# Optimization experiments

Hardware: AMD Instinct MI355X
Metric: run time of the kernel (lower is better)

## Reference

```python
import jax, jax.numpy as jnp
import numpy as np

B, C1, C2, K, H, W = 2, 256, 256, 3, 64, 64
PAD = 1
EPS = 1e-5
K2 = K * K
OUT_OFF = 3 * K2  # deform_groups=1: 2*k2 offset channels + k2 mask channels


def setup_inputs() -> dict:
    key = jax.random.key(0)
    ks = jax.random.split(key, 8)
    x = jax.random.normal(ks[0], (B, C1, H, W), jnp.float32)
    # small scale so predicted offsets stay within a few pixels (realistic trained regime)
    w_off = jax.random.normal(ks[1], (OUT_OFF, C1, 3, 3), jnp.float32) * 0.01
    b_off = jax.random.normal(ks[2], (OUT_OFF,), jnp.float32) * 0.01
    w_dcn = jax.random.normal(ks[3], (C2, C1, K, K), jnp.float32) / np.sqrt(C1 * K2).astype(np.float32)
    gamma = 1.0 + 0.1 * jax.random.normal(ks[4], (C2,), jnp.float32)
    beta = 0.1 * jax.random.normal(ks[5], (C2,), jnp.float32)
    run_mean = 0.1 * jax.random.normal(ks[6], (C2,), jnp.float32)
    run_var = jax.random.uniform(ks[7], (C2,), jnp.float32, minval=0.5, maxval=1.5)
    return {"x": x, "w_off": w_off, "b_off": b_off, "w_dcn": w_dcn,
            "gamma": gamma, "beta": beta, "run_mean": run_mean, "run_var": run_var}


def _dcnv2_bn_silu(x, w_off, b_off, w_dcn, gamma, beta, run_mean, run_var):
    # offset/mask predictor: plain 3x3 conv, stride 1, pad 1
    om = jax.lax.conv_general_dilated(x, w_off, (1, 1), [(PAD, PAD), (PAD, PAD)])
    om = om + b_off[None, :, None, None]  # [B, 27, H, W]
    # mmcv channel layout: (dy, dx) interleaved per kernel tap, then mask
    offset = om[:, :2 * K2].reshape(B, K2, 2, H, W)
    mask = jax.nn.sigmoid(om[:, 2 * K2:3 * K2])  # [B, K2, H, W]
    dy, dx = offset[:, :, 0], offset[:, :, 1]     # [B, K2, H, W]

    ki = jnp.arange(K)
    tap_y = jnp.repeat(ki, K)  # [K2]
    tap_x = jnp.tile(ki, K)    # [K2]
    base_y = jnp.arange(H)[None, None, :, None] - PAD + tap_y[None, :, None, None]
    base_x = jnp.arange(W)[None, None, None, :] - PAD + tap_x[None, :, None, None]
    py = base_y.astype(x.dtype) + dy  # [B, K2, H, W] sampling rows
    px = base_x.astype(x.dtype) + dx  # [B, K2, H, W] sampling cols

    y0f = jnp.floor(py)
    x0f = jnp.floor(px)
    ly = (py - y0f)[:, None]  # [B, 1, K2, H, W]
    lx = (px - x0f)[:, None]
    y0 = y0f.astype(jnp.int32)
    x0 = x0f.astype(jnp.int32)

    x_flat = x.reshape(B, C1, H * W)

    def gather(yi, xi):
        valid = ((yi >= 0) & (yi < H) & (xi >= 0) & (xi < W)).astype(x.dtype)
        idx = jnp.clip(yi, 0, H - 1) * W + jnp.clip(xi, 0, W - 1)  # [B, K2, H, W]
        v = jnp.take_along_axis(x_flat, idx.reshape(B, 1, -1), axis=2)
        return v.reshape(B, C1, K2, H, W) * valid[:, None]

    v00 = gather(y0, x0)
    v01 = gather(y0, x0 + 1)
    v10 = gather(y0 + 1, x0)
    v11 = gather(y0 + 1, x0 + 1)
    vals = (v00 * (1 - ly) * (1 - lx) + v01 * (1 - ly) * lx
            + v10 * ly * (1 - lx) + v11 * ly * lx)
    vals = vals * mask[:, None]  # modulated

    out = jnp.einsum('bckhw,ock->bohw', vals, w_dcn.reshape(C2, C1, K2))

    # BatchNorm (inference, running stats) + SiLU
    inv = gamma / jnp.sqrt(run_var + EPS)
    y = out * inv[None, :, None, None] + (beta - run_mean * inv)[None, :, None, None]
    return y * jax.nn.sigmoid(y)


def reference(x, w_off, b_off, w_dcn, gamma, beta, run_mean, run_var):
    return _dcnv2_bn_silu(x, w_off, b_off, w_dcn, gamma, beta, run_mean, run_var)
```

## Files before the change

kernel.cpp:

```cpp
#include <hip/hip_runtime.h>
#include <hip/hip_bf16.h>
#include <math.h>

typedef __bf16 bf16x8 __attribute__((ext_vector_type(8)));
typedef float  f32x4  __attribute__((ext_vector_type(4)));

#define BB 2
#define C1 256
#define C2 256
#define HH 64
#define WW 64
#define HW 4096
#define OCH 27
#define EPSV 1e-5f

#define OM_OFF   0u
#define WBF_OFF  884736u
#define WOFF_OFF 2064384u
#define XT_OFF   2211840u

__global__ __launch_bounds__(256) void xprep_kernel(
    const float* __restrict__ x, __bf16* __restrict__ xT)
{
    __shared__ __bf16 tile[64][72];

    const int bt = blockIdx.x;
    const int b = bt >> 8;
    const int ht = (bt & 255) >> 2;
    const int ct = bt & 3;
    const int tid = threadIdx.x;

    const int hw_l = tid & 63, cg = tid >> 6;
    const float* src = x + ((size_t)(b * 256 + ct * 64 + cg * 16) << 12) + ht * 64 + hw_l;
    #pragma unroll
    for (int i = 0; i < 16; i++)
        tile[hw_l][cg * 16 + i] = (__bf16)src[(size_t)i << 12];
    __syncthreads();

    const int hw_o = tid >> 2, cq = tid & 3;
    __bf16* dst = xT + ((size_t)(b * HW + ht * 64 + hw_o) << 8) + ct * 64 + cq * 16;
    *(bf16x8*)dst       = *(const bf16x8*)&tile[hw_o][cq * 16];
    *(bf16x8*)(dst + 8) = *(const bf16x8*)&tile[hw_o][cq * 16 + 8];
}

__global__ __launch_bounds__(256) void wprep_kernel(
    const float* __restrict__ w, __bf16* __restrict__ wbfS)
{
    int t = blockIdx.x * 256 + threadIdx.x;
    int l = t & 63;
    int nb = (t >> 6) & 15;
    int ks = (t >> 10) & 1;
    int kb = t >> 11;
    int o = nb * 16 + (l & 15);
    int kq = (l >> 4) & 3;
    bf16x8 v;
    #pragma unroll
    for (int j = 0; j < 8; j++) {
        int K = kb * 64 + ks * 32 + kq * 8 + j;
        v[j] = (__bf16)w[o * 2304 + (K & 255) * 9 + (K >> 8)];
    }
    *(bf16x8*)(wbfS + (size_t)t * 8) = v;
}

__global__ __launch_bounds__(256) void wprep_off_kernel(
    const float* __restrict__ w_off, __bf16* __restrict__ woffS)
{
    int t = blockIdx.x * 256 + threadIdx.x;
    int l = t & 63;
    int nf = (t >> 6) & 1;
    int ks = (t >> 7) & 1;
    int kb = t >> 8;
    int o = nf * 16 + (l & 15);
    int kq = (l >> 4) & 3;
    bf16x8 v;
    #pragma unroll
    for (int j = 0; j < 8; j++) {
        int K = kb * 64 + ks * 32 + kq * 8 + j;
        v[j] = (o < OCH) ? (__bf16)w_off[o * 2304 + (K & 255) * 9 + (K >> 8)]
                         : (__bf16)0.f;
    }
    *(bf16x8*)(woffS + (size_t)t * 8) = v;
}

__global__ __launch_bounds__(256) void offset_mfma_kernel(
    const __bf16* __restrict__ xT, const __bf16* __restrict__ woffS,
    const float* __restrict__ b_off, float* __restrict__ om)
{
    __shared__ float sD[4][16][33];

    const int tid = threadIdx.x, wv = tid >> 6, lane = tid & 63;
    const int g = (blockIdx.x & 7) * 64 + (blockIdx.x >> 3);
    const int pixBase = g * 16;
    const int b = pixBase >> 12;
    const int hwBase = pixBase & 4095;
    const int h = hwBase >> 6, w0 = hwBase & 63;
    const int n15 = lane & 15, q4 = lane >> 4;

    f32x4 acc[2];
    #pragma unroll
    for (int j = 0; j < 2; j++) acc[j] = (f32x4){0.f, 0.f, 0.f, 0.f};

    const char* xb = (const char*)xT + ((size_t)b << 12) * 512;

    for (int i = 0; i < 9; i++) {
        const int kb = wv * 9 + i;
        const int k = kb >> 2, cc = kb & 3;
        const int kh = k / 3, kw = k % 3;
        const int hh = h + kh - 1;
        const int ww = w0 + n15 + kw - 1;
        const bool valid = (hh >= 0) && (hh < HH) && (ww >= 0) && (ww < WW);
        const int hc = min(max(hh, 0), HH - 1);
        const int wc = min(max(ww, 0), WW - 1);
        const char* src = xb + (size_t)(hc * WW + wc) * 512 + (cc * 64 + q4 * 8) * 2;

        bf16x8 af[2];
        af[0] = *(const bf16x8*)src;
        af[1] = *(const bf16x8*)(src + 64);
        if (!valid) {
            #pragma unroll
            for (int j = 0; j < 8; j++) { af[0][j] = (__bf16)0.f; af[1][j] = (__bf16)0.f; }
        }

        #pragma unroll
        for (int nf = 0; nf < 2; nf++) {
            #pragma unroll
            for (int ks = 0; ks < 2; ks++) {
                bf16x8 bfr = *(const bf16x8*)(woffS
                    + ((size_t)(((kb * 2 + ks) * 2 + nf) * 64 + lane)) * 8);
                acc[nf] = __builtin_amdgcn_mfma_f32_16x16x32_bf16(
                    af[ks], bfr, acc[nf], 0, 0, 0);
            }
        }
    }

    #pragma unroll
    for (int nf = 0; nf < 2; nf++)
        #pragma unroll
        for (int r = 0; r < 4; r++)
            sD[wv][q4 * 4 + r][nf * 16 + n15] = acc[nf][r];
    __syncthreads();

    for (int t = tid; t < OCH * 16; t += 256) {
        int oc = t >> 4, m = t & 15;
        float s = b_off[oc] + sD[0][m][oc] + sD[1][m][oc] + sD[2][m][oc] + sD[3][m][oc];
        om[(size_t)b * OCH * HW + oc * HW + hwBase + m] = s;
    }
}

__global__ __launch_bounds__(256) void fused_kernel(
    const __bf16* __restrict__ xT, const float* __restrict__ om,
    const __bf16* __restrict__ wbfS,
    const float* __restrict__ gamma, const float* __restrict__ beta,
    const float* __restrict__ rmean, const float* __restrict__ rvar,
    float* __restrict__ out)
{
    __shared__ int4   sO[9][16];
    __shared__ float4 sW[9][16];
    __shared__ float  sC[2][16][260];

    const int tid = threadIdx.x, wv = tid >> 6, lane = tid & 63;
    const int g = (blockIdx.x & 7) * 64 + (blockIdx.x >> 3);
    const int pixBase = g * 16;
    const int b = pixBase >> 12;
    const int hwBase = pixBase & 4095;
    const int h = hwBase >> 6, w0 = hwBase & 63;

    const float* omb = om + (size_t)b * OCH * HW;
    if (tid < 144) {
        int k = tid >> 4, p = tid & 15;
        int hw = hwBase + p;
        float dy  = omb[(2 * k) * HW + hw];
        float dx  = omb[(2 * k + 1) * HW + hw];
        float mm  = omb[(18 + k) * HW + hw];
        mm = 1.f / (1.f + __expf(-mm));
        float py = (float)(h - 1 + k / 3) + dy;
        float px = (float)(w0 + p - 1 + k % 3) + dx;
        float y0f = floorf(py), x0f = floorf(px);
        float ly = py - y0f, lx = px - x0f;
        int y0 = (int)y0f, x0 = (int)x0f;
        int yc0 = min(max(y0, 0), HH - 1),     yc1 = min(max(y0 + 1, 0), HH - 1);
        int xc0 = min(max(x0, 0), WW - 1),     xc1 = min(max(x0 + 1, 0), WW - 1);
        float vy0 = (y0 >= 0 && y0 < HH) ? 1.f : 0.f;
        float vy1 = (y0 + 1 >= 0 && y0 + 1 < HH) ? 1.f : 0.f;
        float vx0 = (x0 >= 0 && x0 < WW) ? 1.f : 0.f;
        float vx1 = (x0 + 1 >= 0 && x0 + 1 < WW) ? 1.f : 0.f;
        sO[k][p] = (int4){(yc0 * WW + xc0) * 512, (yc0 * WW + xc1) * 512,
                          (yc1 * WW + xc0) * 512, (yc1 * WW + xc1) * 512};
        sW[k][p] = (float4){(1.f - ly) * (1.f - lx) * vy0 * vx0 * mm,
                            (1.f - ly) * lx         * vy0 * vx1 * mm,
                            ly         * (1.f - lx) * vy1 * vx0 * mm,
                            ly         * lx         * vy1 * vx1 * mm};
    }
    __syncthreads();

    const int n15 = lane & 15, q4 = lane >> 4;

    f32x4 acc[16];
    #pragma unroll
    for (int j = 0; j < 16; j++) acc[j] = (f32x4){0.f, 0.f, 0.f, 0.f};

    const char* xb = (const char*)xT + ((size_t)b << 12) * 512;

    for (int i = 0; i < 9; i++) {
        const int kb = wv * 9 + i;
        const int k = kb >> 2, cc = kb & 3;
        const int4   O = sO[k][n15];
        const float4 W = sW[k][n15];
        const char* base = xb + (cc * 64 + q4 * 8) * 2;

        bf16x8 af[2];
        #pragma unroll
        for (int ks = 0; ks < 2; ks++) {
            const char* bc = base + ks * 64;
            bf16x8 c00 = *(const bf16x8*)(bc + O.x);
            bf16x8 c01 = *(const bf16x8*)(bc + O.y);
            bf16x8 c10 = *(const bf16x8*)(bc + O.z);
            bf16x8 c11 = *(const bf16x8*)(bc + O.w);
            bf16x8 a;
            #pragma unroll
            for (int j = 0; j < 8; j++) {
                float v = W.x * (float)c00[j] + W.y * (float)c01[j]
                        + W.z * (float)c10[j] + W.w * (float)c11[j];
                a[j] = (__bf16)v;
            }
            af[ks] = a;
        }

        #pragma unroll
        for (int half = 0; half < 2; half++) {
            bf16x8 bfr[8][2];
            #pragma unroll
            for (int nb = 0; nb < 8; nb++)
                #pragma unroll
                for (int ks = 0; ks < 2; ks++)
                    bfr[nb][ks] = *(const bf16x8*)(wbfS
                        + ((size_t)(((kb * 2 + ks) * 16 + half * 8 + nb) * 64 + lane)) * 8);
            #pragma unroll
            for (int nb = 0; nb < 8; nb++)
                #pragma unroll
                for (int ks = 0; ks < 2; ks++)
                    acc[half * 8 + nb] = __builtin_amdgcn_mfma_f32_16x16x32_bf16(
                        af[ks], bfr[nb][ks], acc[half * 8 + nb], 0, 0, 0);
        }
    }

    if (wv < 2) {
        #pragma unroll
        for (int nb = 0; nb < 16; nb++)
            #pragma unroll
            for (int r = 0; r < 4; r++)
                sC[wv][q4 * 4 + r][nb * 16 + n15] = acc[nb][r];
    }
    __syncthreads();
    if (wv >= 2) {
        #pragma unroll
        for (int nb = 0; nb < 16; nb++)
            #pragma unroll
            for (int r = 0; r < 4; r++)
                sC[wv - 2][q4 * 4 + r][nb * 16 + n15] += acc[nb][r];
    }
    __syncthreads();

    const int px = tid & 15, og = tid >> 4;
    float* ob = out + ((size_t)b * C2 << 12) + hwBase + px;
    #pragma unroll
    for (int ii = 0; ii < 16; ii++) {
        int o = og * 16 + ii;
        float s = sC[0][px][o] + sC[1][px][o];
        float inv = gamma[o] * rsqrtf(rvar[o] + EPSV);
        float sh = beta[o] - rmean[o] * inv;
        float y = s * inv + sh;
        ob[(size_t)o << 12] = y * (1.f / (1.f + __expf(-y)));
    }
}

extern "C" void kernel_launch(void* const* d_in, const int* in_sizes, int n_in,
                              void* d_out, int out_size, void* d_ws, size_t ws_size,
                              hipStream_t stream) {
    const float* x      = (const float*)d_in[0];
    const float* w_off  = (const float*)d_in[1];
    const float* b_off  = (const float*)d_in[2];
    const float* w_dcn  = (const float*)d_in[3];
    const float* gamma  = (const float*)d_in[4];
    const float* beta   = (const float*)d_in[5];
    const float* rmean  = (const float*)d_in[6];
    const float* rvar   = (const float*)d_in[7];
    float* out = (float*)d_out;

    char* ws = (char*)d_ws;
    float*  om    = (float*)(ws + OM_OFF);
    __bf16* wbfS  = (__bf16*)(ws + WBF_OFF);
    __bf16* woffS = (__bf16*)(ws + WOFF_OFF);
    __bf16* xT    = (__bf16*)(ws + XT_OFF);

    xprep_kernel<<<512, 256, 0, stream>>>(x, xT);
    wprep_kernel<<<288, 256, 0, stream>>>(w_dcn, wbfS);
    wprep_off_kernel<<<36, 256, 0, stream>>>(w_off, woffS);
    offset_mfma_kernel<<<512, 256, 0, stream>>>(xT, woffS, b_off, om);
    fused_kernel<<<512, 256, 0, stream>>>(xT, om, wbfS, gamma, beta,
                                          rmean, rvar, out);
}
```

Before: 129.0 us.

## Fuse offset conv into DCN kernel, merge prep kernels, split output channels

Merges the three preprocessing kernels into one launch and folds the offset/mask convolution into the main deformable-conv kernel, keeping offsets in shared memory so the global om buffer round trip and two launches go away. The main kernel now splits the 256 output channels across two blocks per pixel tile, giving 1024 blocks with half the accumulators, and sets a launch-bounds occupancy hint. In exchange, each block recomputes the offset convolution, so that work is done twice per tile.

```diff
diff --git a/kernel.cpp b/kernel.cpp
--- a/kernel.cpp
+++ b/kernel.cpp
@@ -14,164 +14,153 @@
 #define OCH 27
 #define EPSV 1e-5f
 
-#define OM_OFF   0u
-#define WBF_OFF  884736u
-#define WOFF_OFF 2064384u
-#define XT_OFF   2211840u
-
-__global__ __launch_bounds__(256) void xprep_kernel(
-    const float* __restrict__ x, __bf16* __restrict__ xT)
+#define WBF_OFF  0u
+#define WOFF_OFF 1179648u
+#define XT_OFF   1327104u
+
+__global__ __launch_bounds__(256) void prep_kernel(
+    const float* __restrict__ x, const float* __restrict__ w_dcn,
+    const float* __restrict__ w_off, __bf16* __restrict__ xT,
+    __bf16* __restrict__ wbfS, __bf16* __restrict__ woffS)
 {
     __shared__ __bf16 tile[64][72];
-
-    const int bt = blockIdx.x;
-    const int b = bt >> 8;
-    const int ht = (bt & 255) >> 2;
-    const int ct = bt & 3;
-    const int tid = threadIdx.x;
-
-    const int hw_l = tid & 63, cg = tid >> 6;
-    const float* src = x + ((size_t)(b * 256 + ct * 64 + cg * 16) << 12) + ht * 64 + hw_l;
-    #pragma unroll
-    for (int i = 0; i < 16; i++)
-        tile[hw_l][cg * 16 + i] = (__bf16)src[(size_t)i << 12];
-    __syncthreads();
-
-    const int hw_o = tid >> 2, cq = tid & 3;
-    __bf16* dst = xT + ((size_t)(b * HW + ht * 64 + hw_o) << 8) + ct * 64 + cq * 16;
-    *(bf16x8*)dst       = *(const bf16x8*)&tile[hw_o][cq * 16];
-    *(bf16x8*)(dst + 8) = *(const bf16x8*)&tile[hw_o][cq * 16 + 8];
+    const int bi = blockIdx.x, tid = threadIdx.x;
+
+    if (bi < 512) {
+        const int b = bi >> 8;
+        const int ht = (bi & 255) >> 2;
+        const int ct = bi & 3;
+        const int hw_l = tid & 63, cg = tid >> 6;
+        const float* src = x + ((size_t)(b * 256 + ct * 64 + cg * 16) << 12)
+                             + ht * 64 + hw_l;
+        #pragma unroll
+        for (int i = 0; i < 16; i++)
+            tile[hw_l][cg * 16 + i] = (__bf16)src[(size_t)i << 12];
+        __syncthreads();
+        const int hw_o = tid >> 2, cq = tid & 3;
+        __bf16* dst = xT + ((size_t)(b * HW + ht * 64 + hw_o) << 8)
+                         + ct * 64 + cq * 16;
+        *(bf16x8*)dst       = *(const bf16x8*)&tile[hw_o][cq * 16];
+        *(bf16x8*)(dst + 8) = *(const bf16x8*)&tile[hw_o][cq * 16 + 8];
+    } else if (bi < 800) {
+        int t = (bi - 512) * 256 + tid;
+        int l = t & 63;
+        int nb = (t >> 6) & 15;
+        int ks = (t >> 10) & 1;
+        int kb = t >> 11;
+        int o = nb * 16 + (l & 15);
+        int kq = (l >> 4) & 3;
+        bf16x8 v;
+        #pragma unroll
+        for (int j = 0; j < 8; j++) {
+            int K = kb * 64 + ks * 32 + kq * 8 + j;
+            v[j] = (__bf16)w_dcn[o * 2304 + (K & 255) * 9 + (K >> 8)];
+        }
+        *(bf16x8*)(wbfS + (size_t)t * 8) = v;
+    } else {
+        int t = (bi - 800) * 256 + tid;
+        int l = t & 63;
+        int nf = (t >> 6) & 1;
+        int ks = (t >> 7) & 1;
+        int kb = t >> 8;
+        int o = nf * 16 + (l & 15);
+        int kq = (l >> 4) & 3;
+        bf16x8 v;
+        #pragma unroll
+        for (int j = 0; j < 8; j++) {
+            int K = kb * 64 + ks * 32 + kq * 8 + j;
+            v[j] = (o < OCH) ? (__bf16)w_off[o * 2304 + (K & 255) * 9 + (K >> 8)]
+                             : (__bf16)0.f;
+        }
+        *(bf16x8*)(woffS + (size_t)t * 8) = v;
+    }
 }
 
-__global__ __launch_bounds__(256) void wprep_kernel(
-    const float* __restrict__ w, __bf16* __restrict__ wbfS)
+union SU {
+    float sD[4][16][33];
+    float sC[2][16][136];
+};
+
+__global__ __launch_bounds__(256, 4) void fused_kernel(
+    const __bf16* __restrict__ xT, const __bf16* __restrict__ wbfS,
+    const __bf16* __restrict__ woffS, const float* __restrict__ b_off,
+    const float* __restrict__ gamma, const float* __restrict__ beta,
+    const float* __restrict__ rmean, const float* __restrict__ rvar,
+    float* __restrict__ out)
 {
-    int t = blockIdx.x * 256 + threadIdx.x;
-    int l = t & 63;
-    int nb = (t >> 6) & 15;
-    int ks = (t >> 10) & 1;
-    int kb = t >> 11;
-    int o = nb * 16 + (l & 15);
-    int kq = (l >> 4) & 3;
-    bf16x8 v;
-    #pragma unroll
-    for (int j = 0; j < 8; j++) {
-        int K = kb * 64 + ks * 32 + kq * 8 + j;
-        v[j] = (__bf16)w[o * 2304 + (K & 255) * 9 + (K >> 8)];
-    }
-    *(bf16x8*)(wbfS + (size_t)t * 8) = v;
-}
-
-__global__ __launch_bounds__(256) void wprep_off_kernel(
-    const float* __restrict__ w_off, __bf16* __restrict__ woffS)
-{
-    int t = blockIdx.x * 256 + threadIdx.x;
-    int l = t & 63;
-    int nf = (t >> 6) & 1;
-    int ks = (t >> 7) & 1;
-    int kb = t >> 8;
-    int o = nf * 16 + (l & 15);
-    int kq = (l >> 4) & 3;
-    bf16x8 v;
-    #pragma unroll
-    for (int j = 0; j < 8; j++) {
-        int K = kb * 64 + ks * 32 + kq * 8 + j;
-        v[j] = (o < OCH) ? (__bf16)w_off[o * 2304 + (K & 255) * 9 + (K >> 8)]
-                         : (__bf16)0.f;
-    }
-    *(bf16x8*)(woffS + (size_t)t * 8) = v;
-}
-
-__global__ __launch_bounds__(256) void offset_mfma_kernel(
-    const __bf16* __restrict__ xT, const __bf16* __restrict__ woffS,
-    const float* __restrict__ b_off, float* __restrict__ om)
-{
-    __shared__ float sD[4][16][33];
+    __shared__ SU u;
+    __shared__ float  sOm[32][16];
+    __shared__ int4   sO[9][16];
+    __shared__ float4 sW[9][16];
 
     const int tid = threadIdx.x, wv = tid >> 6, lane = tid & 63;
-    const int g = (blockIdx.x & 7) * 64 + (blockIdx.x >> 3);
+    const int bi = blockIdx.x;
+    const int xcd = bi & 7, rr = bi >> 3;
+    const int g = xcd * 64 + (rr >> 1);
+    const int nHalf = rr & 1;
     const int pixBase = g * 16;
     const int b = pixBase >> 12;
     const int hwBase = pixBase & 4095;
     const int h = hwBase >> 6, w0 = hwBase & 63;
     const int n15 = lane & 15, q4 = lane >> 4;
 
-    f32x4 acc[2];
-    #pragma unroll
-    for (int j = 0; j < 2; j++) acc[j] = (f32x4){0.f, 0.f, 0.f, 0.f};
-
     const char* xb = (const char*)xT + ((size_t)b << 12) * 512;
 
-    for (int i = 0; i < 9; i++) {
-        const int kb = wv * 9 + i;
-        const int k = kb >> 2, cc = kb & 3;
-        const int kh = k / 3, kw = k % 3;
-        const int hh = h + kh - 1;
-        const int ww = w0 + n15 + kw - 1;
-        const bool valid = (hh >= 0) && (hh < HH) && (ww >= 0) && (ww < WW);
-        const int hc = min(max(hh, 0), HH - 1);
-        const int wc = min(max(ww, 0), WW - 1);
-        const char* src = xb + (size_t)(hc * WW + wc) * 512 + (cc * 64 + q4 * 8) * 2;
-
-        bf16x8 af[2];
-        af[0] = *(const bf16x8*)src;
-        af[1] = *(const bf16x8*)(src + 64);
-        if (!valid) {
-            #pragma unroll
-            for (int j = 0; j < 8; j++) { af[0][j] = (__bf16)0.f; af[1][j] = (__bf16)0.f; }
-        }
-
-        #pragma unroll
-        for (int nf = 0; nf < 2; nf++) {
-            #pragma unroll
-            for (int ks = 0; ks < 2; ks++) {
-                bf16x8 bfr = *(const bf16x8*)(woffS
-                    + ((size_t)(((kb * 2 + ks) * 2 + nf) * 64 + lane)) * 8);
-                acc[nf] = __builtin_amdgcn_mfma_f32_16x16x32_bf16(
-                    af[ks], bfr, acc[nf], 0, 0, 0);
+    {
+        f32x4 acc2[2];
+        #pragma unroll
+        for (int j = 0; j < 2; j++) acc2[j] = (f32x4){0.f, 0.f, 0.f, 0.f};
+
+        for (int i = 0; i < 9; i++) {
+            const int kb = wv * 9 + i;
+            const int k = kb >> 2, cc = kb & 3;
+            const int kh = k / 3, kw = k % 3;
+            const int hh = h + kh - 1;
+            const int ww = w0 + n15 + kw - 1;
+            const bool valid = (hh >= 0) && (hh < HH) && (ww >= 0) && (ww < WW);
+            const int hc = min(max(hh, 0), HH - 1);
+            const int wc = min(max(ww, 0), WW - 1);
+            const char* src = xb + (size_t)(hc * WW + wc) * 512
+                                 + (cc * 64 + q4 * 8) * 2;
+            bf16x8 af[2];
+            af[0] = *(const bf16x8*)src;
+            af[1] = *(const bf16x8*)(src + 64);
+            if (!valid) {
+                #pragma unroll
+                for (int j = 0; j < 8; j++) {
+                    af[0][j] = (__bf16)0.f; af[1][j] = (__bf16)0.f;
+                }
             }
-        }
-    }
-
-    #pragma unroll
-    for (int nf = 0; nf < 2; nf++)
-        #pragma unroll
-        for (int r = 0; r < 4; r++)
-            sD[wv][q4 * 4 + r][nf * 16 + n15] = acc[nf][r];
-    __syncthreads();
-
+            #pragma unroll
+            for (int nf = 0; nf < 2; nf++) {
+                #pragma unroll
+                for (int ks = 0; ks < 2; ks++) {
+                    bf16x8 bfr = *(const bf16x8*)(woffS
+                        + ((size_t)(((kb * 2 + ks) * 2 + nf) * 64 + lane)) * 8);
+                    acc2[nf] = __builtin_amdgcn_mfma_f32_16x16x32_bf16(
+                        af[ks], bfr, acc2[nf], 0, 0, 0);
+                }
+            }
+        }
+        #pragma unroll
+        for (int nf = 0; nf < 2; nf++)
+            #pragma unroll
+            for (int r = 0; r < 4; r++)
+                u.sD[wv][q4 * 4 + r][nf * 16 + n15] = acc2[nf][r];
+    }
+    __syncthreads();
     for (int t = tid; t < OCH * 16; t += 256) {
-        int oc = t >> 4, m = t & 15;
-        float s = b_off[oc] + sD[0][m][oc] + sD[1][m][oc] + sD[2][m][oc] + sD[3][m][oc];
-        om[(size_t)b * OCH * HW + oc * HW + hwBase + m] = s;
-    }
-}
-
-__global__ __launch_bounds__(256) void fused_kernel(
-    const __bf16* __restrict__ xT, const float* __restrict__ om,
-    const __bf16* __restrict__ wbfS,
-    const float* __restrict__ gamma, const float* __restrict__ beta,
-    const float* __restrict__ rmean, const float* __restrict__ rvar,
-    float* __restrict__ out)
-{
-    __shared__ int4   sO[9][16];
-    __shared__ float4 sW[9][16];
-    __shared__ float  sC[2][16][260];
-
-    const int tid = threadIdx.x, wv = tid >> 6, lane = tid & 63;
-    const int g = (blockIdx.x & 7) * 64 + (blockIdx.x >> 3);
-    const int pixBase = g * 16;
-    const int b = pixBase >> 12;
-    const int hwBase = pixBase & 4095;
-    const int h = hwBase >> 6, w0 = hwBase & 63;
-
-    const float* omb = om + (size_t)b * OCH * HW;
+        int oc = t >> 4, p = t & 15;
+        sOm[oc][p] = b_off[oc] + u.sD[0][p][oc] + u.sD[1][p][oc]
+                               + u.sD[2][p][oc] + u.sD[3][p][oc];
+    }
+    __syncthreads();
+
     if (tid < 144) {
         int k = tid >> 4, p = tid & 15;
-        int hw = hwBase + p;
-        float dy  = omb[(2 * k) * HW + hw];
-        float dx  = omb[(2 * k + 1) * HW + hw];
-        float mm  = omb[(18 + k) * HW + hw];
+        float dy = sOm[2 * k][p];
+        float dx = sOm[2 * k + 1][p];
+        float mm = sOm[18 + k][p];
         mm = 1.f / (1.f + __expf(-mm));
         float py = (float)(h - 1 + k / 3) + dy;
         float px = (float)(w0 + p - 1 + k % 3) + dx;
@@ -193,13 +182,9 @@
     }
     __syncthreads();
 
-    const int n15 = lane & 15, q4 = lane >> 4;
-
-    f32x4 acc[16];
+    f32x4 acc[8];
     #pragma unroll
-    for (int j = 0; j < 16; j++) acc[j] = (f32x4){0.f, 0.f, 0.f, 0.f};
-
-    const char* xb = (const char*)xT + ((size_t)b << 12) * 512;
+    for (int j = 0; j < 8; j++) acc[j] = (f32x4){0.f, 0.f, 0.f, 0.f};
 
     for (int i = 0; i < 9; i++) {
         const int kb = wv * 9 + i;
@@ -228,45 +213,47 @@
 
         #pragma unroll
         for (int half = 0; half < 2; half++) {
-            bf16x8 bfr[8][2];
-            #pragma unroll
-            for (int nb = 0; nb < 8; nb++)
+            bf16x8 bfr[4][2];
+            #pragma unroll
+            for (int nb = 0; nb < 4; nb++)
                 #pragma unroll
                 for (int ks = 0; ks < 2; ks++)
                     bfr[nb][ks] = *(const bf16x8*)(wbfS
-                        + ((size_t)(((kb * 2 + ks) * 16 + half * 8 + nb) * 64 + lane)) * 8);
-            #pragma unroll
-            for (int nb = 0; nb < 8; nb++)
+                        + ((size_t)(((kb * 2 + ks) * 16 + nHalf * 8 + half * 4 + nb)
+                                    * 64 + lane)) * 8);
+            #pragma unroll
+            for (int nb = 0; nb < 4; nb++)
                 #pragma unroll
                 for (int ks = 0; ks < 2; ks++)
-                    acc[half * 8 + nb] = __builtin_amdgcn_mfma_f32_16x16x32_bf16(
-                        af[ks], bfr[nb][ks], acc[half * 8 + nb], 0, 0, 0);
+                    acc[half * 4 + nb] = __builtin_amdgcn_mfma_f32_16x16x32_bf16(
+                        af[ks], bfr[nb][ks], acc[half * 4 + nb], 0, 0, 0);
         }
     }
 
     if (wv < 2) {
         #pragma unroll
-        for (int nb = 0; nb < 16; nb++)
+        for (int nb = 0; nb < 8; nb++)
             #pragma unroll
             for (int r = 0; r < 4; r++)
-                sC[wv][q4 * 4 + r][nb * 16 + n15] = acc[nb][r];
+                u.sC[wv][q4 * 4 + r][nb * 16 + n15] = acc[nb][r];
     }
     __syncthreads();
     if (wv >= 2) {
         #pragma unroll
-        for (int nb = 0; nb < 16; nb++)
+        for (int nb = 0; nb < 8; nb++)
             #pragma unroll
             for (int r = 0; r < 4; r++)
-                sC[wv - 2][q4 * 4 + r][nb * 16 + n15] += acc[nb][r];
+                u.sC[wv - 2][q4 * 4 + r][nb * 16 + n15] += acc[nb][r];
     }
     __syncthreads();
 
     const int px = tid & 15, og = tid >> 4;
     float* ob = out + ((size_t)b * C2 << 12) + hwBase + px;
     #pragma unroll
-    for (int ii = 0; ii < 16; ii++) {
-        int o = og * 16 + ii;
-        float s = sC[0][px][o] + sC[1][px][o];
+    for (int ii = 0; ii < 8; ii++) {
+        int col = og * 8 + ii;
+        int o = nHalf * 128 + col;
+        float s = u.sC[0][px][col] + u.sC[1][px][col];
         float inv = gamma[o] * rsqrtf(rvar[o] + EPSV);
         float sh = beta[o] - rmean[o] * inv;
         float y = s * inv + sh;
@@ -288,15 +275,11 @@
     float* out = (float*)d_out;
 
     char* ws = (char*)d_ws;
-    float*  om    = (float*)(ws + OM_OFF);
     __bf16* wbfS  = (__bf16*)(ws + WBF_OFF);
     __bf16* woffS = (__bf16*)(ws + WOFF_OFF);
     __bf16* xT    = (__bf16*)(ws + XT_OFF);
 
-    xprep_kernel<<<512, 256, 0, stream>>>(x, xT);
-    wprep_kernel<<<288, 256, 0, stream>>>(w_dcn, wbfS);
-    wprep_off_kernel<<<36, 256, 0, stream>>>(w_off, woffS);
-    offset_mfma_kernel<<<512, 256, 0, stream>>>(xT, woffS, b_off, om);
-    fused_kernel<<<512, 256, 0, stream>>>(xT, om, wbfS, gamma, beta,
-                                          rmean, rvar, out);
+    prep_kernel<<<836, 256, 0, stream>>>(x, w_dcn, w_off, xT, wbfS, woffS);
+    fused_kernel<<<1024, 256, 0, stream>>>(xT, wbfS, woffS, b_off,
+                                           gamma, beta, rmean, rvar, out);
 }
```

After: 141.5 us. 9.6% more time.
